# Performance work log

Measured on AMD Instinct MI355X. Metric: run time of the kernel, lower is better.

## Reference

```python
import jax, jax.numpy as jnp
import numpy as np

K, STRIDE, PAD = 3, 1, 1


def _unfold(x, k=K, stride=STRIDE, pad=PAD):
    # x: [B, C, H, W] -> patches [B, C*k*k, L] (im2col, torch nn.Unfold layout:
    # channel index = c*k*k + ki*k + kj)
    p = jax.lax.conv_general_dilated_patches(
        x, filter_shape=(k, k), window_strides=(stride, stride),
        padding=((pad, pad), (pad, pad)))  # [B, C*k*k, Ho, Wo]
    B = x.shape[0]
    return p.reshape(B, p.shape[1], -1)


def reference(x, weight, dweight, bias):
    B, C, H, W = x.shape
    O = weight.shape[0]
    cols = _unfold(x)                                   # [B, C*k*k, L]
    # scalar gate per spatial position: dweight . sigmoid(cols)
    gate = jnp.einsum('f,bfl->bl', dweight.reshape(-1), jax.nn.sigmoid(cols))
    gated = cols * gate[:, None, :]                     # [B, C*k*k, L]
    out = jnp.einsum('of,bfl->bol', weight.reshape(O, -1), gated)  # [B, O, L]
    out = out + bias[None, :, None]
    Ho, Wo = (H // 2, W // 2) if STRIDE == 2 else (H, W)
    return out.reshape(B, O, Ho, Wo)


def setup_inputs() -> dict:
    key = jax.random.key(0)
    k1, k2, k3, k4 = jax.random.split(key, 4)
    B, C, O, H, W = 8, 32, 32, 256, 256
    fan_out = O * K * K
    std = float(np.sqrt(2.0 / fan_out))
    return {
        'x': jax.random.normal(k1, (B, C, H, W), dtype=jnp.float32),
        'weight': jax.random.normal(k2, (O, C, K, K), dtype=jnp.float32) * std,
        'dweight': jax.random.normal(k3, (1, C, K, K), dtype=jnp.float32) * std,
        'bias': jax.random.normal(k4, (O,), dtype=jnp.float32),
    }
```

## Files before the change

### kernel.cpp

```cpp
#include <hip/hip_runtime.h>


typedef _Float16 half8 __attribute__((ext_vector_type(8)));
typedef _Float16 half4 __attribute__((ext_vector_type(4)));
typedef float f32x16 __attribute__((ext_vector_type(16)));

#define BATCH 8
#define CIN 32
#define COUT 32
#define HH 256
#define WW 256
#define TW 32
#define TH 8
#define HTW 34
#define HTH 10
#define CSTR 40
#define NCHUNK 18
#define NPOS (HTH*HTW)
#define NITEM (NPOS*8)

__global__ __launch_bounds__(256) void prep_pack(const float* __restrict__ w,
                                                 const float* __restrict__ dw,
                                                 _Float16* __restrict__ Apack,
                                                 float* __restrict__ dwf) {
  int t = blockIdx.x * 256 + threadIdx.x;
  if (t < 9216) {
    int q = t >> 9, lane = (t >> 3) & 63, j = t & 7;
    int tap = q >> 1, h = q & 1;
    int o = lane & 31, lh = lane >> 5;
    int c = h * 16 + lh * 8 + j;
    Apack[t] = (_Float16)w[o * 288 + c * 9 + tap];
  } else if (t < 9216 + 288) {
    int i = t - 9216;
    int tap = i >> 5, c = i & 31;
    dwf[i] = dw[c * 9 + tap];
  }
}

__global__ __launch_bounds__(512, 4) void dynconv(
    const float* __restrict__ x, const _Float16* __restrict__ Apack,
    const float* __restrict__ dwf, const float* __restrict__ bias,
    float* __restrict__ out) {
  __shared__ __align__(16) _Float16 lv[NPOS * CSTR];
  __shared__ float gpart[9 * NPOS];

  const int bid0 = blockIdx.x;
  const int bb = bid0 & 7, idx = bid0 >> 3;
  const int xt = idx & 7, yt = idx >> 3;
  const int x0 = xt * TW, y0 = yt * TH;
  const int tid = threadIdx.x;

  for (int i = tid; i < NITEM; i += 512) {
    const int cg = i / NPOS;
    const int pos = i - cg * NPOS;
    const int yy = pos / HTW;
    const int xx = pos - yy * HTW;
    const int gy = y0 + yy - 1, gx = x0 + xx - 1;
    float v0 = 0.f, v1 = 0.f, v2 = 0.f, v3 = 0.f;
    if ((unsigned)gy < 256u && (unsigned)gx < 256u) {
      const float* xp = x + (((size_t)(bb * CIN + cg * 4)) << 16) + (gy << 8) + gx;
      v0 = xp[0]; v1 = xp[1 << 16]; v2 = xp[2 << 16]; v3 = xp[3 << 16];
    }
    half4 hv = {(_Float16)v0, (_Float16)v1, (_Float16)v2, (_Float16)v3};
    *(half4*)(lv + pos * CSTR + cg * 4) = hv;
  }
  __syncthreads();

  if (tid < NPOS) {
    const _Float16* base = lv + tid * CSTR;
    float p[9];
#pragma unroll
    for (int tap = 0; tap < 9; ++tap) p[tap] = 0.f;
    for (int c = 0; c < CIN; ++c) {
      const float v = (float)base[c];
      const float s = __builtin_amdgcn_rcpf(1.f + __expf(-v));
#pragma unroll
      for (int tap = 0; tap < 9; ++tap)
        p[tap] += dwf[tap * 32 + c] * s;
    }
#pragma unroll
    for (int tap = 0; tap < 9; ++tap)
      gpart[tap * NPOS + tid] = p[tap];
  }
  __syncthreads();

  const int lane = tid & 63, w8 = tid >> 6;
  const int ln = lane & 31, lh = lane >> 5;

  float gate = 0.f;
#pragma unroll
  for (int ki = 0; ki < 3; ++ki)
#pragma unroll
    for (int kj = 0; kj < 3; ++kj)
      gate += gpart[(ki * 3 + kj) * NPOS + (w8 + ki) * HTW + ln + kj];

  f32x16 acc;
#pragma unroll
  for (int i = 0; i < 16; ++i) acc[i] = 0.f;

#pragma unroll
  for (int q = 0; q < NCHUNK; ++q) {
    const int tap = q >> 1, h = q & 1;
    const int ki = tap / 3, kj = tap - ki * 3;
    const half8 a = *(const half8*)(Apack + ((q * 64 + lane) << 3));
    const int off = ((w8 + ki) * HTW + ln + kj) * CSTR + h * 16 + lh * 8;
    const half8 bv = *(const half8*)(lv + off);
    acc = __builtin_amdgcn_mfma_f32_32x32x16_f16(a, bv, acc, 0, 0, 0);
  }

  const int y = y0 + w8;
#pragma unroll
  for (int reg = 0; reg < 16; ++reg) {
    const int o = (reg & 3) + 8 * (reg >> 2) + 4 * lh;
    out[(((size_t)(bb * COUT + o)) << 16) + (y << 8) + x0 + ln] =
        acc[reg] * gate + bias[o];
  }
}

extern "C" void kernel_launch(void* const* d_in, const int* in_sizes, int n_in,
                              void* d_out, int out_size, void* d_ws, size_t ws_size,
                              hipStream_t stream) {
  const float* x    = (const float*)d_in[0];
  const float* wgt  = (const float*)d_in[1];
  const float* dw   = (const float*)d_in[2];
  const float* bias = (const float*)d_in[3];
  float* out = (float*)d_out;

  _Float16* Apack = (_Float16*)d_ws;
  float* dwf      = (float*)((char*)d_ws + 18432);

  prep_pack<<<(9216 + 288 + 255) / 256, 256, 0, stream>>>(wgt, dw, Apack, dwf);
  dynconv<<<BATCH * (HH / TH) * (WW / TW), 512, 0, stream>>>(x, Apack, dwf, bias, out);
}
```

Before: 144.6 us.

## Halve tile height and fuse halo load with sigmoid-gate computation per thread

Shrinks the tile from 8 to 4 output rows, giving 256-thread blocks with a different occupancy hint. Each of 204 threads now loads all 32 channels of one halo position into registers, computes the sigmoid-weighted partial gates directly from fp32 values, and writes the fp16 row to LDS with vector stores. This drops one barrier and the LDS round trip before the gate step. In exchange the halo overhead per output grows (6 rows loaded for 4), about 52 threads idle during the load, and each thread carries more registers.

```diff
diff --git a/kernel.cpp b/kernel.cpp
--- a/kernel.cpp
+++ b/kernel.cpp
@@ -2,7 +2,6 @@
 
 
 typedef _Float16 half8 __attribute__((ext_vector_type(8)));
-typedef _Float16 half4 __attribute__((ext_vector_type(4)));
 typedef float f32x16 __attribute__((ext_vector_type(16)));
 
 #define BATCH 8
@@ -11,13 +10,12 @@
 #define HH 256
 #define WW 256
 #define TW 32
-#define TH 8
+#define TH 4
 #define HTW 34
-#define HTH 10
+#define HTH 6
 #define CSTR 40
 #define NCHUNK 18
 #define NPOS (HTH*HTW)
-#define NITEM (NPOS*8)
 
 __global__ __launch_bounds__(256) void prep_pack(const float* __restrict__ w,
                                                  const float* __restrict__ dw,
@@ -37,7 +35,7 @@
   }
 }
 
-__global__ __launch_bounds__(512, 4) void dynconv(
+__global__ __launch_bounds__(256, 6) void dynconv(
     const float* __restrict__ x, const _Float16* __restrict__ Apack,
     const float* __restrict__ dwf, const float* __restrict__ bias,
     float* __restrict__ out) {
@@ -50,34 +48,34 @@
   const int x0 = xt * TW, y0 = yt * TH;
   const int tid = threadIdx.x;
 
-  for (int i = tid; i < NITEM; i += 512) {
-    const int cg = i / NPOS;
-    const int pos = i - cg * NPOS;
-    const int yy = pos / HTW;
-    const int xx = pos - yy * HTW;
+  if (tid < NPOS) {
+    const int yy = tid / HTW, xx = tid - (tid / HTW) * HTW;
     const int gy = y0 + yy - 1, gx = x0 + xx - 1;
-    float v0 = 0.f, v1 = 0.f, v2 = 0.f, v3 = 0.f;
+    const int voff = (gy << 8) + gx;
+    float v[CIN];
     if ((unsigned)gy < 256u && (unsigned)gx < 256u) {
-      const float* xp = x + (((size_t)(bb * CIN + cg * 4)) << 16) + (gy << 8) + gx;
-      v0 = xp[0]; v1 = xp[1 << 16]; v2 = xp[2 << 16]; v3 = xp[3 << 16];
+#pragma unroll
+      for (int c = 0; c < CIN; ++c)
+        v[c] = x[(((size_t)(bb * CIN + c)) << 16) + voff];
+    } else {
+#pragma unroll
+      for (int c = 0; c < CIN; ++c) v[c] = 0.f;
     }
-    half4 hv = {(_Float16)v0, (_Float16)v1, (_Float16)v2, (_Float16)v3};
-    *(half4*)(lv + pos * CSTR + cg * 4) = hv;
-  }
-  __syncthreads();
-
-  if (tid < NPOS) {
-    const _Float16* base = lv + tid * CSTR;
     float p[9];
 #pragma unroll
     for (int tap = 0; tap < 9; ++tap) p[tap] = 0.f;
+    _Float16 hv[CIN];
+#pragma unroll
     for (int c = 0; c < CIN; ++c) {
-      const float v = (float)base[c];
-      const float s = __builtin_amdgcn_rcpf(1.f + __expf(-v));
+      const float s = __builtin_amdgcn_rcpf(1.f + __expf(-v[c]));
 #pragma unroll
       for (int tap = 0; tap < 9; ++tap)
         p[tap] += dwf[tap * 32 + c] * s;
+      hv[c] = (_Float16)v[c];
     }
+#pragma unroll
+    for (int u = 0; u < 4; ++u)
+      *(half8*)(lv + tid * CSTR + u * 8) = *(const half8*)(hv + u * 8);
 #pragma unroll
     for (int tap = 0; tap < 9; ++tap)
       gpart[tap * NPOS + tid] = p[tap];
@@ -108,12 +106,11 @@
     acc = __builtin_amdgcn_mfma_f32_32x32x16_f16(a, bv, acc, 0, 0, 0);
   }
 
-  const int y = y0 + w8;
+  const int voff_out = ((y0 + w8) << 8) + x0 + ln;
 #pragma unroll
   for (int reg = 0; reg < 16; ++reg) {
     const int o = (reg & 3) + 8 * (reg >> 2) + 4 * lh;
-    out[(((size_t)(bb * COUT + o)) << 16) + (y << 8) + x0 + ln] =
-        acc[reg] * gate + bias[o];
+    out[(((size_t)(bb * COUT + o)) << 16) + voff_out] = acc[reg] * gate + bias[o];
   }
 }
 
@@ -130,5 +127,5 @@
   float* dwf      = (float*)((char*)d_ws + 18432);
 
   prep_pack<<<(9216 + 288 + 255) / 256, 256, 0, stream>>>(wgt, dw, Apack, dwf);
-  dynconv<<<BATCH * (HH / TH) * (WW / TW), 512, 0, stream>>>(x, Apack, dwf, bias, out);
+  dynconv<<<BATCH * (HH / TH) * (WW / TW), 256, 0, stream>>>(x, Apack, dwf, bias, out);
 }
```

After: 133.8 us. 7.5% less time.
